# Performance work log

Hardware: AMD Instinct MI355X
Metric: run time of the kernel (lower is better)

Reference implementation:

```python
import jax, jax.numpy as jnp
import numpy as np

# __init__ constants of RMSELoss(early, gap, late)
EARLY = 1
GAP = 0.5
LATE = 2


def setup_inputs() -> dict:
    key = jax.random.key(0)
    k1, k2 = jax.random.split(key)
    N = 16777216  # rows; column dim is 1 since forward indexes inputs[r, 0]
    inputs = jax.random.normal(k1, (N, 1), dtype=jnp.float32)
    targets = jax.random.normal(k2, (N, 1), dtype=jnp.float32)
    return {"inputs": inputs, "targets": targets}


def reference(inputs, targets):
    # train=True path of RMSELoss.forward, fully vectorized.
    d = targets - inputs  # [N, 1]
    # per-row weight: 2+early if d>=gap, 2+late if d<0, else 0 (d**0 == 1,
    # including 0**0 == 1, matching torch.pow semantics).
    early_term = d ** (2 + EARLY)  # integer_pow handles negative bases exactly
    late_term = d ** (2 + LATE)
    v = jnp.where(d >= GAP, early_term,
                  jnp.where(d < 0, late_term, jnp.ones_like(d)))
    return jnp.mean(v) ** 0.5
```

## Files before the change

### kernel.cpp

```cpp
#include <hip/hip_runtime.h>
#include <math.h>


#define BLOCK  256
#define UNROLL 8
#define NWAVE  (BLOCK / 64)

typedef float vfloat4 __attribute__((ext_vector_type(4)));

__device__ __forceinline__ float vfun(float d) {
    float d2 = d * d;
    float e  = d2 * d;
    float l  = d2 * d2;
    return d >= 0.5f ? e : (d < 0.0f ? l : 1.0f);
}

__device__ __forceinline__ float vfun4(vfloat4 a, vfloat4 b) {
    return vfun(b.x - a.x) + vfun(b.y - a.y) + vfun(b.z - a.z) + vfun(b.w - a.w);
}

__global__ __launch_bounds__(BLOCK) void rmse_partial(
        const vfloat4* __restrict__ x4,
        const vfloat4* __restrict__ t4,
        const float*  __restrict__ x,
        const float*  __restrict__ t,
        float* __restrict__ block_sums,
        int n4, int n) {
    const int chunk = BLOCK * UNROLL;
    int base = blockIdx.x * chunk + threadIdx.x;

    float acc0 = 0.0f, acc1 = 0.0f, acc2 = 0.0f, acc3 = 0.0f;

    if ((blockIdx.x + 1) * chunk <= n4) {
        vfloat4 a[UNROLL], b[UNROLL];
        #pragma unroll
        for (int j = 0; j < UNROLL; ++j) {
            a[j] = __builtin_nontemporal_load(&x4[base + j * BLOCK]);
            b[j] = __builtin_nontemporal_load(&t4[base + j * BLOCK]);
        }
        acc0 += vfun4(a[0], b[0]);
        acc1 += vfun4(a[1], b[1]);
        acc2 += vfun4(a[2], b[2]);
        acc3 += vfun4(a[3], b[3]);
        acc0 += vfun4(a[4], b[4]);
        acc1 += vfun4(a[5], b[5]);
        acc2 += vfun4(a[6], b[6]);
        acc3 += vfun4(a[7], b[7]);
    } else {
        #pragma unroll
        for (int j = 0; j < UNROLL; ++j) {
            int i = base + j * BLOCK;
            if (i < n4)
                acc0 += vfun4(__builtin_nontemporal_load(&x4[i]),
                              __builtin_nontemporal_load(&t4[i]));
        }
    }
    if (blockIdx.x == 0 && threadIdx.x == 0) {
        for (int j = n4 * 4; j < n; ++j) acc0 += vfun(t[j] - x[j]);
    }

    float acc = (acc0 + acc1) + (acc2 + acc3);

    #pragma unroll
    for (int off = 32; off > 0; off >>= 1)
        acc += __shfl_down(acc, off, 64);

    __shared__ float smem[NWAVE];
    int lane = threadIdx.x & 63;
    int wave = threadIdx.x >> 6;
    if (lane == 0) smem[wave] = acc;
    __syncthreads();
    if (threadIdx.x == 0) {
        float s = 0.0f;
        #pragma unroll
        for (int w = 0; w < NWAVE; ++w) s += smem[w];
        block_sums[blockIdx.x] = s;
    }
}

__global__ __launch_bounds__(1024) void rmse_final(
        const float* __restrict__ block_sums,
        float* __restrict__ out, float inv_n, int nb) {
    float s = 0.0f;
    for (int i = threadIdx.x; i < nb; i += 1024) s += block_sums[i];

    #pragma unroll
    for (int off = 32; off > 0; off >>= 1)
        s += __shfl_down(s, off, 64);

    __shared__ float smem[16];
    int lane = threadIdx.x & 63;
    int wave = threadIdx.x >> 6;
    if (lane == 0) smem[wave] = s;
    __syncthreads();
    if (threadIdx.x == 0) {
        float tot = 0.0f;
        #pragma unroll
        for (int w = 0; w < 16; ++w) tot += smem[w];
        out[0] = sqrtf(tot * inv_n);
    }
}

extern "C" void kernel_launch(void* const* d_in, const int* in_sizes, int n_in,
                              void* d_out, int out_size, void* d_ws, size_t ws_size,
                              hipStream_t stream) {
    const float* x = (const float*)d_in[0];
    const float* t = (const float*)d_in[1];
    float* out = (float*)d_out;
    float* ws  = (float*)d_ws;

    int n  = in_sizes[0];
    int n4 = n / 4;

    const int chunk = BLOCK * UNROLL;
    int grid = (n4 + chunk - 1) / chunk;

    rmse_partial<<<grid, BLOCK, 0, stream>>>(
        (const vfloat4*)x, (const vfloat4*)t, x, t, ws, n4, n);

    rmse_final<<<1, 1024, 0, stream>>>(ws, out, 1.0f / (float)n, grid);
}
```

Baseline: 137.5 us.

## Fuse partial and final reduction into one cooperative persistent kernel

Replaces the two-kernel reduction with a single cooperative, grid-stride persistent kernel. It writes per-block partials, does a grid-wide sync, and lets block 0 compute the final sqrt of the mean. The aim is to remove the second kernel launch and the tail of a very large grid, with occupancy sizing the grid. It also halves the unroll factor, and the grid barrier adds a synchronisation cost of its own. The old two-kernel path stays as a fallback.

```diff
diff --git a/kernel.cpp b/kernel.cpp
--- a/kernel.cpp
+++ b/kernel.cpp
@@ -1,10 +1,13 @@
 #include <hip/hip_runtime.h>
+#include <hip/hip_cooperative_groups.h>
 #include <math.h>
 
 
 #define BLOCK  256
-#define UNROLL 8
+#define UNROLL 4
 #define NWAVE  (BLOCK / 64)
+
+namespace cg = cooperative_groups;
 
 typedef float vfloat4 __attribute__((ext_vector_type(4)));
 
@@ -17,6 +20,83 @@
 
 __device__ __forceinline__ float vfun4(vfloat4 a, vfloat4 b) {
     return vfun(b.x - a.x) + vfun(b.y - a.y) + vfun(b.z - a.z) + vfun(b.w - a.w);
+}
+
+__global__ __launch_bounds__(BLOCK) void rmse_fused(
+        const vfloat4* __restrict__ x4,
+        const vfloat4* __restrict__ t4,
+        const float*  __restrict__ x,
+        const float*  __restrict__ t,
+        float* __restrict__ ws,
+        float* __restrict__ out,
+        float inv_n, int n4, int n, int nchunks) {
+    const int chunk = BLOCK * UNROLL;
+    float acc0 = 0.0f, acc1 = 0.0f, acc2 = 0.0f, acc3 = 0.0f;
+
+    for (int c = blockIdx.x; c < nchunks; c += gridDim.x) {
+        int base = c * chunk + threadIdx.x;
+        if ((c + 1) * chunk <= n4) {
+            vfloat4 a[UNROLL], b[UNROLL];
+            #pragma unroll
+            for (int j = 0; j < UNROLL; ++j) {
+                a[j] = __builtin_nontemporal_load(&x4[base + j * BLOCK]);
+                b[j] = __builtin_nontemporal_load(&t4[base + j * BLOCK]);
+            }
+            acc0 += vfun4(a[0], b[0]);
+            acc1 += vfun4(a[1], b[1]);
+            acc2 += vfun4(a[2], b[2]);
+            acc3 += vfun4(a[3], b[3]);
+        } else {
+            #pragma unroll
+            for (int j = 0; j < UNROLL; ++j) {
+                int i = base + j * BLOCK;
+                if (i < n4)
+                    acc0 += vfun4(__builtin_nontemporal_load(&x4[i]),
+                                  __builtin_nontemporal_load(&t4[i]));
+            }
+        }
+    }
+    if (blockIdx.x == 0 && threadIdx.x == 0) {
+        for (int j = n4 * 4; j < n; ++j) acc0 += vfun(t[j] - x[j]);
+    }
+
+    float acc = (acc0 + acc1) + (acc2 + acc3);
+
+    #pragma unroll
+    for (int off = 32; off > 0; off >>= 1)
+        acc += __shfl_down(acc, off, 64);
+
+    __shared__ float smem[NWAVE];
+    int lane = threadIdx.x & 63;
+    int wave = threadIdx.x >> 6;
+    if (lane == 0) smem[wave] = acc;
+    __syncthreads();
+    if (threadIdx.x == 0) {
+        float s = 0.0f;
+        #pragma unroll
+        for (int w = 0; w < NWAVE; ++w) s += smem[w];
+        ws[blockIdx.x] = s;
+    }
+
+    cg::this_grid().sync();
+
+    if (blockIdx.x == 0) {
+        float s = 0.0f;
+        for (int i = threadIdx.x; i < (int)gridDim.x; i += BLOCK)
+            s += ws[i];
+        #pragma unroll
+        for (int off = 32; off > 0; off >>= 1)
+            s += __shfl_down(s, off, 64);
+        __syncthreads();
+        if (lane == 0) smem[wave] = s;
+        __syncthreads();
+        if (threadIdx.x == 0) {
+            float tot = 0.0f;
+            #pragma unroll
+            for (int w = 0; w < NWAVE; ++w) tot += smem[w];
+            out[0] = sqrtf(tot * inv_n);
+        }
+    }
 }
 
 __global__ __launch_bounds__(BLOCK) void rmse_partial(
@@ -29,7 +109,7 @@
     const int chunk = BLOCK * UNROLL;
     int base = blockIdx.x * chunk + threadIdx.x;
 
-    float acc0 = 0.0f, acc1 = 0.0f, acc2 = 0.0f, acc3 = 0.0f;
+    float acc0 = 0.0f, acc1 = 0.0f;
 
     if ((blockIdx.x + 1) * chunk <= n4) {
         vfloat4 a[UNROLL], b[UNROLL];
@@ -40,12 +120,8 @@
         }
         acc0 += vfun4(a[0], b[0]);
         acc1 += vfun4(a[1], b[1]);
-        acc2 += vfun4(a[2], b[2]);
-        acc3 += vfun4(a[3], b[3]);
-        acc0 += vfun4(a[4], b[4]);
-        acc1 += vfun4(a[5], b[5]);
-        acc2 += vfun4(a[6], b[6]);
-        acc3 += vfun4(a[7], b[7]);
+        acc0 += vfun4(a[2], b[2]);
+        acc1 += vfun4(a[3], b[3]);
     } else {
         #pragma unroll
         for (int j = 0; j < UNROLL; ++j) {
@@ -59,7 +135,7 @@
         for (int j = n4 * 4; j < n; ++j) acc0 += vfun(t[j] - x[j]);
     }
 
-    float acc = (acc0 + acc1) + (acc2 + acc3);
+    float acc = acc0 + acc1;
 
     #pragma unroll
     for (int off = 32; off > 0; off >>= 1)
@@ -113,10 +189,40 @@
     int n4 = n / 4;
 
     const int chunk = BLOCK * UNROLL;
-    int grid = (n4 + chunk - 1) / chunk;
-
-    rmse_partial<<<grid, BLOCK, 0, stream>>>(
-        (const vfloat4*)x, (const vfloat4*)t, x, t, ws, n4, n);
-
-    rmse_final<<<1, 1024, 0, stream>>>(ws, out, 1.0f / (float)n, grid);
-}
+    int nchunks = (n4 + chunk - 1) / chunk;
+    float inv_n = 1.0f / (float)n;
+
+    static int coop_grid = -1;
+    if (coop_grid < 0) {
+        int dev = 0;
+        hipGetDevice(&dev);
+        hipDeviceProp_t prop;
+        if (hipGetDeviceProperties(&prop, dev) == hipSuccess) {
+            int mb = 0;
+            if (hipOccupancyMaxActiveBlocksPerMultiprocessor(
+                    &mb, (const void*)rmse_fused, BLOCK, 0) == hipSuccess && mb > 0)
+                coop_grid = mb * prop.multiProcessorCount;
+        }
+        if (coop_grid <= 0) coop_grid = 0;
+    }
+
+    bool launched = false;
+    if (coop_grid > 0) {
+        int grid = nchunks < coop_grid ? nchunks : coop_grid;
+        const vfloat4* x4p = (const vfloat4*)x;
+        const vfloat4* t4p = (const vfloat4*)t;
+        void* args[] = { (void*)&x4p, (void*)&t4p, (void*)&x, (void*)&t,
+                         (void*)&ws, (void*)&out, (void*)&inv_n,
+                         (void*)&n4, (void*)&n, (void*)&nchunks };
+        hipError_t e = hipLaunchCooperativeKernel(
+            (const void*)rmse_fused, dim3(grid), dim3(BLOCK), args, 0, stream);
+        launched = (e == hipSuccess);
+        if (!launched) coop_grid = 0;
+    }
+
+    if (!launched) {
+        rmse_partial<<<nchunks, BLOCK, 0, stream>>>(
+            (const vfloat4*)x, (const vfloat4*)t, x, t, ws, n4, n);
+        rmse_final<<<1, 1024, 0, stream>>>(ws, out, inv_n, nchunks);
+    }
+}
```

Measured after the change: 282.6 us. +105.5%, slower.
